# Optimization experiments

Hardware: AMD Instinct MI355X
Metric: run time of the kernel (lower is better)

Reference implementation:

```python
import jax, jax.numpy as jnp
import numpy as np

B, K, H, W, N = 256, 16, 64, 64, 1024   # batch, channels (n_ch), grid H/W, sampled sites
F_IN = 9 * K - 1                         # 3x3 neighborhood * K channels, minus center channel


def setup_inputs() -> dict:
    key = jax.random.key(0)
    ks = jax.random.split(key, 8)
    z_int = jax.random.randint(ks[0], (B, K, H, W), 0, 16, dtype=jnp.int32)
    bs = jax.random.randint(ks[1], (N,), 0, K, dtype=jnp.int32)
    ii = jax.random.randint(ks[2], (N,), 0, H, dtype=jnp.int32)
    jj = jax.random.randint(ks[3], (N,), 0, W, dtype=jnp.int32)
    W1 = jax.random.normal(ks[4], (F_IN, 128), dtype=jnp.float32) * 0.05
    b1 = jnp.zeros((128,), dtype=jnp.float32)
    W2 = jax.random.normal(ks[5], (128, 16), dtype=jnp.float32) * 0.05
    b2 = jnp.zeros((16,), dtype=jnp.float32)
    return {"z_int": z_int, "bs": bs, "ii": ii, "jj": jj,
            "W1": W1, "b1": b1, "W2": W2, "b2": b2}


def _gather_ctx(z_f, bs, ii, jj):
    # Faithful to get_context ordering: loops di, dj (each in [-1,0,1]) then b,
    # skipping (di==0, dj==0, b==bi). Flattened skip position = 4*K + bi.
    off = jnp.array([-1, 0, 1], dtype=jnp.int32)
    di = jnp.repeat(off, 3)          # [9]
    dj = jnp.tile(off, 3)            # [9]
    ni = (ii[:, None] + di[None, :]) % H   # [N, 9] toroidal wrap
    nj = (jj[:, None] + dj[None, :]) % W   # [N, 9]
    ctx = z_f[:, :, ni, nj]                # [B, K, N, 9]
    ctx = jnp.transpose(ctx, (2, 0, 3, 1)).reshape(N, B, 9 * K)  # [N, B, 9K], (di,dj) major then b
    drop = 4 * K + bs                      # [N] center-channel flat index
    idx = jnp.arange(F_IN, dtype=jnp.int32)
    keep = idx[None, :] + (idx[None, :] >= drop[:, None]).astype(jnp.int32)  # [N, F_IN]
    return jax.vmap(lambda c, k: c[:, k])(ctx, keep)  # [N, B, F_IN]


def reference(z_int, bs, ii, jj, W1, b1, W2, b2):
    z_f = z_int.astype(jnp.float32) / 15.0
    ctx = _gather_ctx(z_f, bs, ii, jj)                 # [N, B, 9K-1]
    h = jax.nn.relu(jnp.einsum('nbf,fh->nbh', ctx, W1) + b1)
    logits = jnp.einsum('nbh,hc->nbc', h, W2) + b2     # [N, B, 16]
    pred = jnp.argmax(logits, axis=-1)                 # [N, B]
    tgt = z_int[:, bs, ii, jj].T                       # [N, B]
    rate = jnp.mean((pred != tgt).astype(jnp.float32)) # np.mean of per-site mean == global mean
    return rate
```

## Files before the change

kernel.cpp:

```cpp
#include <hip/hip_runtime.h>
#include <stdint.h>

#define NB 1024
#define BB 256
#define KK 16
#define HH 64
#define WW 64
#define F_FULL 144
#define HDIM 128
#define CDIM 16
#define KPAD 160
#define APITCH 168
#define HPITCH 136
#define ABYTES (64 * APITCH * 2)

typedef __bf16 bf16x8 __attribute__((ext_vector_type(8)));
typedef float f32x4 __attribute__((ext_vector_type(4)));

#define W1T_OFF 256
#define W1T_BYTES (16 * HDIM * KPAD * 2)
#define W2B_OFF (W1T_OFF + W1T_BYTES)
#define W2B_BYTES (CDIM * HDIM * 2)
#define ZT_OFF (W2B_OFF + W2B_BYTES)

__device__ __forceinline__ unsigned short bf16_bits(float v) {
    __bf16 b = (__bf16)v;
    return __builtin_bit_cast(unsigned short, b);
}

#define TP 144
__global__ __launch_bounds__(256) void prep_kernel(
    const int* __restrict__ z, const float* __restrict__ W1,
    const float* __restrict__ W2, uint8_t* __restrict__ zt,
    unsigned short* __restrict__ W1t, unsigned short* __restrict__ W2b,
    int* __restrict__ counters) {
    int bid = blockIdx.x;
    int t = threadIdx.x;
    if (bid < 4096) {
        __shared__ uint8_t tile[32 * TP];
        int bx = bid & 127;
        int by = bid >> 7;
        int c0 = bx * 32, r0 = by * 128;
#pragma unroll
        for (int i = 0; i < 4; ++i) {
            int lin = i * 256 + t;
            int c = lin & 31;
            int rq = lin >> 5;
            uchar4 v;
            v.x = (uint8_t)z[(size_t)(r0 + rq * 4 + 0) * 4096 + c0 + c];
            v.y = (uint8_t)z[(size_t)(r0 + rq * 4 + 1) * 4096 + c0 + c];
            v.z = (uint8_t)z[(size_t)(r0 + rq * 4 + 2) * 4096 + c0 + c];
            v.w = (uint8_t)z[(size_t)(r0 + rq * 4 + 3) * 4096 + c0 + c];
            *(uchar4*)(tile + c * TP + rq * 4) = v;
        }
        __syncthreads();
        int cy = t >> 3, rx = t & 7;
        uint4 v = *(const uint4*)(tile + cy * TP + rx * 16);
        *(uint4*)(zt + (size_t)(c0 + cy) * 4096 + r0 + rx * 16) = v;
    } else if (bid < 5376) {
        int idx = (bid - 4096) * 256 + t;
        int k = idx % KPAD;
        int h = (idx / KPAD) % HDIM;
        int s = idx / (KPAD * HDIM);
        int drop = 4 * KK + s;
        float val = 0.0f;
        if (k < F_FULL && k != drop) {
            int src = k - (k > drop ? 1 : 0);
            val = W1[src * HDIM + h];
        }
        W1t[idx] = bf16_bits(val);
    } else {
        int idx = (bid - 5376) * 256 + t;
        if (idx < CDIM * HDIM) {
            int k = idx % HDIM;
            int c = idx / HDIM;
            W2b[idx] = bf16_bits(W2[k * CDIM + c]);
        }
        if (bid == 5376 && t == 0) counters[0] = 0;
    }
}

__global__ __launch_bounds__(256, 3) void main_kernel(
    const uint8_t* __restrict__ zt, const unsigned short* __restrict__ W1t,
    const float* __restrict__ b1, const unsigned short* __restrict__ W2b,
    const float* __restrict__ b2, const int* __restrict__ bs,
    const int* __restrict__ ii, const int* __restrict__ jj,
    int* __restrict__ counters) {
    __shared__ __align__(16) unsigned char smem[2 * ABYTES + 64 * 17 * 4];
    unsigned short* sA0 = (unsigned short*)smem;
    unsigned short* sA1 = (unsigned short*)(smem + ABYTES);
    float* slg = (float*)(smem + 2 * ABYTES);

    int t = threadIdx.x;
    int n = blockIdx.x;
    int wave = t >> 6, lane = t & 63;
    int l15 = lane & 15, l4 = lane >> 4;

    int in_ = ii[n], jn = jj[n], sn = bs[n];

    const unsigned short* w1s = W1t + (size_t)sn * (HDIM * KPAD);
    int n0 = wave * 32;
    bf16x8 Bf[2][5];
#pragma unroll
    for (int nt = 0; nt < 2; ++nt)
#pragma unroll
        for (int ks = 0; ks < 5; ++ks)
            Bf[nt][ks] = *(const bf16x8*)(w1s + (n0 + nt * 16 + l15) * KPAD + ks * 32 + l4 * 8);
    bf16x8 Bf2[4];
#pragma unroll
    for (int ks = 0; ks < 4; ++ks)
        Bf2[ks] = *(const bf16x8*)(W2b + l15 * HDIM + ks * 32 + l4 * 8);
    float b1v0 = b1[n0 + l15], b1v1 = b1[n0 + 16 + l15];
    float b2v = b2[l15];

    if (t < 192) {
        int b = t / 3, part = t % 3;
        *(uint4*)(sA0 + b * APITCH + F_FULL + part * 8) = make_uint4(0, 0, 0, 0);
        *(uint4*)(sA1 + b * APITCH + F_FULL + part * 8) = make_uint4(0, 0, 0, 0);
    }

    uint4 g0, g1, g2;
    auto gload = [&](int tile) {
        int b = (t & 63) + tile * 64;
        int p0 = t >> 6;
        int ni0 = (in_ + p0 / 3 - 1) & (HH - 1);
        int nj0 = (jn + p0 % 3 - 1) & (WW - 1);
        g0 = *(const uint4*)(zt + (((size_t)(ni0 * WW + nj0) * BB + b) << 4));
        int p1 = p0 + 4;
        int ni1 = (in_ + p1 / 3 - 1) & (HH - 1);
        int nj1 = (jn + p1 % 3 - 1) & (WW - 1);
        g1 = *(const uint4*)(zt + (((size_t)(ni1 * WW + nj1) * BB + b) << 4));
        if (t < 64) {
            int ni2 = (in_ + 1) & (HH - 1);
            int nj2 = (jn + 1) & (WW - 1);
            g2 = *(const uint4*)(zt + (((size_t)(ni2 * WW + nj2) * BB + b) << 4));
        }
    };
    auto gwrite = [&](unsigned short* dst) {
        int b = t & 63;
        int p0 = t >> 6;
        auto conv = [&](uint4 raw, int p) {
            const uint8_t* bytes = (const uint8_t*)&raw;
            union { __bf16 h[16]; uint4 q[2]; } u;
#pragma unroll
            for (int k = 0; k < 16; ++k)
                u.h[k] = (__bf16)((float)bytes[k] * (1.0f / 15.0f));
            uint4* d = (uint4*)(dst + b * APITCH + p * 16);
            d[0] = u.q[0];
            d[1] = u.q[1];
        };
        conv(g0, p0);
        conv(g1, p0 + 4);
        if (t < 64) conv(g2, 8);
    };

    gload(0);
    gwrite(sA0);
    int local_err = 0;

    for (int tile = 0; tile < 4; ++tile) {
        unsigned short* sA = (tile & 1) ? sA1 : sA0;
        unsigned short* sH = sA;
        unsigned short* sAnext = (tile & 1) ? sA0 : sA1;

        if (tile < 3) gload(tile + 1);
        __syncthreads();

        f32x4 acc[4][2] = {};
#pragma unroll
        for (int mt = 0; mt < 4; ++mt) {
            bf16x8 Af[5];
#pragma unroll
            for (int ks = 0; ks < 5; ++ks)
                Af[ks] = *(const bf16x8*)(sA + (mt * 16 + l15) * APITCH + ks * 32 + l4 * 8);
#pragma unroll
            for (int ks = 0; ks < 5; ++ks) {
                acc[mt][0] = __builtin_amdgcn_mfma_f32_16x16x32_bf16(Af[ks], Bf[0][ks], acc[mt][0], 0, 0, 0);
                acc[mt][1] = __builtin_amdgcn_mfma_f32_16x16x32_bf16(Af[ks], Bf[1][ks], acc[mt][1], 0, 0, 0);
            }
        }
        __syncthreads();

#pragma unroll
        for (int mt = 0; mt < 4; ++mt)
#pragma unroll
            for (int nt = 0; nt < 2; ++nt) {
                float bv = nt ? b1v1 : b1v0;
                int hcol = n0 + nt * 16 + l15;
#pragma unroll
                for (int r = 0; r < 4; ++r) {
                    int b = mt * 16 + l4 * 4 + r;
                    float v = fmaxf(acc[mt][nt][r] + bv, 0.0f);
                    sH[b * HPITCH + hcol] = bf16_bits(v);
                }
            }
        __syncthreads();

        f32x4 acc2 = {};
#pragma unroll
        for (int ks = 0; ks < 4; ++ks) {
            bf16x8 Af = *(const bf16x8*)(sH + (wave * 16 + l15) * HPITCH + ks * 32 + l4 * 8);
            acc2 = __builtin_amdgcn_mfma_f32_16x16x32_bf16(Af, Bf2[ks], acc2, 0, 0, 0);
        }
#pragma unroll
        for (int r = 0; r < 4; ++r) {
            int b = wave * 16 + l4 * 4 + r;
            slg[b * 17 + l15] = acc2[r] + b2v;
        }
        __syncthreads();

        if (t < 64) {
            float best = slg[t * 17];
            int pi = 0;
#pragma unroll
            for (int c = 1; c < CDIM; ++c) {
                float v = slg[t * 17 + c];
                if (v > best) { best = v; pi = c; }
            }
            int bglob = tile * 64 + t;
            int tgt = zt[(((size_t)(in_ * WW + jn) * BB + bglob) << 4) + sn];
            unsigned long long m = __ballot(pi != tgt);
            if (t == 0) local_err += (int)__popcll(m);
        }
        if (tile < 3) gwrite(sAnext);
    }

    if (t == 0) atomicAdd(&counters[0], local_err);
}

__global__ void finalize_kernel(const int* __restrict__ counters, float* __restrict__ out) {
    out[0] = (float)(counters[0]) / (float)(NB * BB);
}

extern "C" void kernel_launch(void* const* d_in, const int* in_sizes, int n_in,
                              void* d_out, int out_size, void* d_ws, size_t ws_size,
                              hipStream_t stream) {
    const int* z = (const int*)d_in[0];
    const int* bs = (const int*)d_in[1];
    const int* ii = (const int*)d_in[2];
    const int* jj = (const int*)d_in[3];
    const float* W1 = (const float*)d_in[4];
    const float* b1 = (const float*)d_in[5];
    const float* W2 = (const float*)d_in[6];
    const float* b2 = (const float*)d_in[7];
    float* out = (float*)d_out;

    uint8_t* ws = (uint8_t*)d_ws;
    int* counters = (int*)ws;
    unsigned short* W1t = (unsigned short*)(ws + W1T_OFF);
    unsigned short* W2b = (unsigned short*)(ws + W2B_OFF);
    uint8_t* zt = ws + ZT_OFF;

    prep_kernel<<<5384, 256, 0, stream>>>(z, W1, W2, zt, W1t, W2b, counters);
    main_kernel<<<NB, 256, 0, stream>>>(zt, W1t, b1, W2b, b2, bs, ii, jj, counters);
    finalize_kernel<<<1, 1, 0, stream>>>(counters, out);
}
```

Measured before the change: 132.7 us.

## Fuse finalize into main kernel, shuffle-based argmax, separate hidden buffer

Drops the separate finalize launch: the last block to finish, found through an atomic ticket counter, writes the output. The argmax over the 16 logits becomes a wave-level shuffle reduction, removing the logits shared-memory round trip and two block barriers per tile. A dedicated shared hidden-activation buffer removes one more barrier. Weight loads are moved after the first gather is issued so their latency overlaps, and the A pitch shrinks to 160, which may add LDS bank conflicts.

```diff
diff --git a/kernel.cpp b/kernel.cpp
--- a/kernel.cpp
+++ b/kernel.cpp
@@ -10,7 +10,7 @@
 #define HDIM 128
 #define CDIM 16
 #define KPAD 160
-#define APITCH 168
+#define APITCH 160
 #define HPITCH 136
 #define ABYTES (64 * APITCH * 2)
 
@@ -76,7 +76,7 @@
             int c = idx / HDIM;
             W2b[idx] = bf16_bits(W2[k * CDIM + c]);
         }
-        if (bid == 5376 && t == 0) counters[0] = 0;
+        if (bid == 5376 && t == 0) { counters[0] = 0; counters[1] = 0; }
     }
 }
 
@@ -85,11 +85,11 @@
     const float* __restrict__ b1, const unsigned short* __restrict__ W2b,
     const float* __restrict__ b2, const int* __restrict__ bs,
     const int* __restrict__ ii, const int* __restrict__ jj,
-    int* __restrict__ counters) {
-    __shared__ __align__(16) unsigned char smem[2 * ABYTES + 64 * 17 * 4];
+    int* __restrict__ counters, float* __restrict__ out) {
+    __shared__ __align__(16) unsigned char smem[2 * ABYTES + 64 * HPITCH * 2];
     unsigned short* sA0 = (unsigned short*)smem;
     unsigned short* sA1 = (unsigned short*)(smem + ABYTES);
-    float* slg = (float*)(smem + 2 * ABYTES);
+    unsigned short* sH = (unsigned short*)(smem + 2 * ABYTES);
 
     int t = threadIdx.x;
     int n = blockIdx.x;
@@ -97,27 +97,6 @@
     int l15 = lane & 15, l4 = lane >> 4;
 
     int in_ = ii[n], jn = jj[n], sn = bs[n];
-
-    const unsigned short* w1s = W1t + (size_t)sn * (HDIM * KPAD);
-    int n0 = wave * 32;
-    bf16x8 Bf[2][5];
-#pragma unroll
-    for (int nt = 0; nt < 2; ++nt)
-#pragma unroll
-        for (int ks = 0; ks < 5; ++ks)
-            Bf[nt][ks] = *(const bf16x8*)(w1s + (n0 + nt * 16 + l15) * KPAD + ks * 32 + l4 * 8);
-    bf16x8 Bf2[4];
-#pragma unroll
-    for (int ks = 0; ks < 4; ++ks)
-        Bf2[ks] = *(const bf16x8*)(W2b + l15 * HDIM + ks * 32 + l4 * 8);
-    float b1v0 = b1[n0 + l15], b1v1 = b1[n0 + 16 + l15];
-    float b2v = b2[l15];
-
-    if (t < 192) {
-        int b = t / 3, part = t % 3;
-        *(uint4*)(sA0 + b * APITCH + F_FULL + part * 8) = make_uint4(0, 0, 0, 0);
-        *(uint4*)(sA1 + b * APITCH + F_FULL + part * 8) = make_uint4(0, 0, 0, 0);
-    }
 
     uint4 g0, g1, g2;
     auto gload = [&](int tile) {
@@ -155,12 +134,32 @@
     };
 
     gload(0);
+
+    const unsigned short* w1s = W1t + (size_t)sn * (HDIM * KPAD);
+    int n0 = wave * 32;
+    bf16x8 Bf[2][5];
+#pragma unroll
+    for (int nt = 0; nt < 2; ++nt)
+#pragma unroll
+        for (int ks = 0; ks < 5; ++ks)
+            Bf[nt][ks] = *(const bf16x8*)(w1s + (n0 + nt * 16 + l15) * KPAD + ks * 32 + l4 * 8);
+    bf16x8 Bf2[4];
+#pragma unroll
+    for (int ks = 0; ks < 4; ++ks)
+        Bf2[ks] = *(const bf16x8*)(W2b + l15 * HDIM + ks * 32 + l4 * 8);
+    float b1v0 = b1[n0 + l15], b1v1 = b1[n0 + 16 + l15];
+    float b2v = b2[l15];
+
+    if (t < 128) {
+        unsigned short* buf = (t & 64) ? sA1 : sA0;
+        *(uint4*)(buf + (t & 63) * APITCH + F_FULL) = make_uint4(0, 0, 0, 0);
+    }
+
     gwrite(sA0);
-    int local_err = 0;
+    int werr = 0;
 
     for (int tile = 0; tile < 4; ++tile) {
         unsigned short* sA = (tile & 1) ? sA1 : sA0;
-        unsigned short* sH = sA;
         unsigned short* sAnext = (tile & 1) ? sA0 : sA1;
 
         if (tile < 3) gload(tile + 1);
@@ -179,7 +178,6 @@
                 acc[mt][1] = __builtin_amdgcn_mfma_f32_16x16x32_bf16(Af[ks], Bf[1][ks], acc[mt][1], 0, 0, 0);
             }
         }
-        __syncthreads();
 
 #pragma unroll
         for (int mt = 0; mt < 4; ++mt)
@@ -202,34 +200,40 @@
             bf16x8 Af = *(const bf16x8*)(sH + (wave * 16 + l15) * HPITCH + ks * 32 + l4 * 8);
             acc2 = __builtin_amdgcn_mfma_f32_16x16x32_bf16(Af, Bf2[ks], acc2, 0, 0, 0);
         }
+
 #pragma unroll
         for (int r = 0; r < 4; ++r) {
-            int b = wave * 16 + l4 * 4 + r;
-            slg[b * 17 + l15] = acc2[r] + b2v;
-        }
-        __syncthreads();
-
-        if (t < 64) {
-            float best = slg[t * 17];
-            int pi = 0;
-#pragma unroll
-            for (int c = 1; c < CDIM; ++c) {
-                float v = slg[t * 17 + c];
-                if (v > best) { best = v; pi = c; }
-            }
-            int bglob = tile * 64 + t;
-            int tgt = zt[(((size_t)(in_ * WW + jn) * BB + bglob) << 4) + sn];
-            unsigned long long m = __ballot(pi != tgt);
-            if (t == 0) local_err += (int)__popcll(m);
-        }
+            float v = acc2[r] + b2v;
+            int idx = l15;
+#pragma unroll
+            for (int off = 1; off < 16; off <<= 1) {
+                float ov = __shfl_xor(v, off);
+                int oi = __shfl_xor(idx, off);
+                if (ov > v || (ov == v && oi < idx)) { v = ov; idx = oi; }
+            }
+            if (l15 == 0) {
+                int bglob = tile * 64 + wave * 16 + l4 * 4 + r;
+                int tgt = zt[(((size_t)(in_ * WW + jn) * BB + bglob) << 4) + sn];
+                werr += (idx != tgt) ? 1 : 0;
+            }
+        }
+
         if (tile < 3) gwrite(sAnext);
     }
 
-    if (t == 0) atomicAdd(&counters[0], local_err);
-}
-
-__global__ void finalize_kernel(const int* __restrict__ counters, float* __restrict__ out) {
-    out[0] = (float)(counters[0]) / (float)(NB * BB);
+#pragma unroll
+    for (int off = 32; off > 0; off >>= 1) werr += __shfl_xor(werr, off);
+    if (lane == 0) atomicAdd(&counters[0], werr);
+
+    __syncthreads();
+    if (t == 0) {
+        __threadfence();
+        int old = atomicAdd(&counters[1], 1);
+        if (old == NB - 1) {
+            int total = atomicAdd(&counters[0], 0);
+            out[0] = (float)total / (float)(NB * BB);
+        }
+    }
 }
 
 extern "C" void kernel_launch(void* const* d_in, const int* in_sizes, int n_in,
@@ -252,6 +256,5 @@
     uint8_t* zt = ws + ZT_OFF;
 
     prep_kernel<<<5384, 256, 0, stream>>>(z, W1, W2, zt, W1t, W2b, counters);
-    main_kernel<<<NB, 256, 0, stream>>>(zt, W1t, b1, W2b, b2, bs, ii, jj, counters);
-    finalize_kernel<<<1, 1, 0, stream>>>(counters, out);
-}
+    main_kernel<<<NB, 256, 0, stream>>>(zt, W1t, b1, W2b, b2, bs, ii, jj, counters, out);
+}
```

Result: slower. 190.2 us (+43.3%).

## Split main kernel across eight waves with one hidden-column tile each

Applied to the files above, without the earlier changes.

Doubles the block to 512 threads so each of the eight waves computes 16 hidden columns of the first GEMM instead of 32. The 3x3 neighborhood gather is spread so each thread loads a single position, and the launch bound moves to (512, 6) to cut per-thread register pressure and raise the number of resident waves. In exchange, the second GEMM runs on only half the waves, and W2 fragments are now reloaded from global memory every tile instead of being held in registers.

```diff
diff --git a/kernel.cpp b/kernel.cpp
--- a/kernel.cpp
+++ b/kernel.cpp
@@ -80,7 +80,7 @@
     }
 }
 
-__global__ __launch_bounds__(256, 3) void main_kernel(
+__global__ __launch_bounds__(512, 6) void main_kernel(
     const uint8_t* __restrict__ zt, const unsigned short* __restrict__ W1t,
     const float* __restrict__ b1, const unsigned short* __restrict__ W2b,
     const float* __restrict__ b2, const int* __restrict__ bs,
@@ -98,38 +98,13 @@
 
     int in_ = ii[n], jn = jj[n], sn = bs[n];
 
-    const unsigned short* w1s = W1t + (size_t)sn * (HDIM * KPAD);
-    int n0 = wave * 32;
-    bf16x8 Bf[2][5];
-#pragma unroll
-    for (int nt = 0; nt < 2; ++nt)
-#pragma unroll
-        for (int ks = 0; ks < 5; ++ks)
-            Bf[nt][ks] = *(const bf16x8*)(w1s + (n0 + nt * 16 + l15) * KPAD + ks * 32 + l4 * 8);
-    bf16x8 Bf2[4];
-#pragma unroll
-    for (int ks = 0; ks < 4; ++ks)
-        Bf2[ks] = *(const bf16x8*)(W2b + l15 * HDIM + ks * 32 + l4 * 8);
-    float b1v0 = b1[n0 + l15], b1v1 = b1[n0 + 16 + l15];
-    float b2v = b2[l15];
-
-    if (t < 192) {
-        int b = t / 3, part = t % 3;
-        *(uint4*)(sA0 + b * APITCH + F_FULL + part * 8) = make_uint4(0, 0, 0, 0);
-        *(uint4*)(sA1 + b * APITCH + F_FULL + part * 8) = make_uint4(0, 0, 0, 0);
-    }
-
-    uint4 g0, g1, g2;
+    uint4 g0, g2;
     auto gload = [&](int tile) {
         int b = (t & 63) + tile * 64;
         int p0 = t >> 6;
         int ni0 = (in_ + p0 / 3 - 1) & (HH - 1);
         int nj0 = (jn + p0 % 3 - 1) & (WW - 1);
         g0 = *(const uint4*)(zt + (((size_t)(ni0 * WW + nj0) * BB + b) << 4));
-        int p1 = p0 + 4;
-        int ni1 = (in_ + p1 / 3 - 1) & (HH - 1);
-        int nj1 = (jn + p1 % 3 - 1) & (WW - 1);
-        g1 = *(const uint4*)(zt + (((size_t)(ni1 * WW + nj1) * BB + b) << 4));
         if (t < 64) {
             int ni2 = (in_ + 1) & (HH - 1);
             int nj2 = (jn + 1) & (WW - 1);
@@ -150,11 +125,26 @@
             d[1] = u.q[1];
         };
         conv(g0, p0);
-        conv(g1, p0 + 4);
         if (t < 64) conv(g2, 8);
     };
 
     gload(0);
+
+    const unsigned short* w1s = W1t + (size_t)sn * (HDIM * KPAD);
+    int n0 = wave * 16;
+    bf16x8 Bf[5];
+#pragma unroll
+    for (int ks = 0; ks < 5; ++ks)
+        Bf[ks] = *(const bf16x8*)(w1s + (n0 + l15) * KPAD + ks * 32 + l4 * 8);
+    float b1v = b1[n0 + l15];
+    float b2v = b2[l15];
+
+    if (t < 192) {
+        int b = t / 3, part = t % 3;
+        *(uint4*)(sA0 + b * APITCH + F_FULL + part * 8) = make_uint4(0, 0, 0, 0);
+        *(uint4*)(sA1 + b * APITCH + F_FULL + part * 8) = make_uint4(0, 0, 0, 0);
+    }
+
     gwrite(sA0);
     int local_err = 0;
 
@@ -166,7 +156,7 @@
         if (tile < 3) gload(tile + 1);
         __syncthreads();
 
-        f32x4 acc[4][2] = {};
+        f32x4 acc[4] = {};
 #pragma unroll
         for (int mt = 0; mt < 4; ++mt) {
             bf16x8 Af[5];
@@ -174,38 +164,33 @@
             for (int ks = 0; ks < 5; ++ks)
                 Af[ks] = *(const bf16x8*)(sA + (mt * 16 + l15) * APITCH + ks * 32 + l4 * 8);
 #pragma unroll
-            for (int ks = 0; ks < 5; ++ks) {
-                acc[mt][0] = __builtin_amdgcn_mfma_f32_16x16x32_bf16(Af[ks], Bf[0][ks], acc[mt][0], 0, 0, 0);
-                acc[mt][1] = __builtin_amdgcn_mfma_f32_16x16x32_bf16(Af[ks], Bf[1][ks], acc[mt][1], 0, 0, 0);
-            }
+            for (int ks = 0; ks < 5; ++ks)
+                acc[mt] = __builtin_amdgcn_mfma_f32_16x16x32_bf16(Af[ks], Bf[ks], acc[mt], 0, 0, 0);
         }
         __syncthreads();
 
 #pragma unroll
         for (int mt = 0; mt < 4; ++mt)
 #pragma unroll
-            for (int nt = 0; nt < 2; ++nt) {
-                float bv = nt ? b1v1 : b1v0;
-                int hcol = n0 + nt * 16 + l15;
-#pragma unroll
-                for (int r = 0; r < 4; ++r) {
-                    int b = mt * 16 + l4 * 4 + r;
-                    float v = fmaxf(acc[mt][nt][r] + bv, 0.0f);
-                    sH[b * HPITCH + hcol] = bf16_bits(v);
-                }
-            }
-        __syncthreads();
-
-        f32x4 acc2 = {};
-#pragma unroll
-        for (int ks = 0; ks < 4; ++ks) {
-            bf16x8 Af = *(const bf16x8*)(sH + (wave * 16 + l15) * HPITCH + ks * 32 + l4 * 8);
-            acc2 = __builtin_amdgcn_mfma_f32_16x16x32_bf16(Af, Bf2[ks], acc2, 0, 0, 0);
-        }
-#pragma unroll
-        for (int r = 0; r < 4; ++r) {
-            int b = wave * 16 + l4 * 4 + r;
-            slg[b * 17 + l15] = acc2[r] + b2v;
+            for (int r = 0; r < 4; ++r) {
+                int b = mt * 16 + l4 * 4 + r;
+                sH[b * HPITCH + n0 + l15] = bf16_bits(fmaxf(acc[mt][r] + b1v, 0.0f));
+            }
+        __syncthreads();
+
+        if (wave < 4) {
+            f32x4 acc2 = {};
+#pragma unroll
+            for (int ks = 0; ks < 4; ++ks) {
+                bf16x8 B2k = *(const bf16x8*)(W2b + l15 * HDIM + ks * 32 + l4 * 8);
+                bf16x8 Af = *(const bf16x8*)(sH + (wave * 16 + l15) * HPITCH + ks * 32 + l4 * 8);
+                acc2 = __builtin_amdgcn_mfma_f32_16x16x32_bf16(Af, B2k, acc2, 0, 0, 0);
+            }
+#pragma unroll
+            for (int r = 0; r < 4; ++r) {
+                int b = wave * 16 + l4 * 4 + r;
+                slg[b * 17 + l15] = acc2[r] + b2v;
+            }
         }
         __syncthreads();
 
@@ -222,6 +207,7 @@
             unsigned long long m = __ballot(pi != tgt);
             if (t == 0) local_err += (int)__popcll(m);
         }
+
         if (tile < 3) gwrite(sAnext);
     }
 
@@ -252,6 +238,6 @@
     uint8_t* zt = ws + ZT_OFF;
 
     prep_kernel<<<5384, 256, 0, stream>>>(z, W1, W2, zt, W1t, W2b, counters);
-    main_kernel<<<NB, 256, 0, stream>>>(zt, W1t, b1, W2b, b2, bs, ii, jj, counters);
+    main_kernel<<<NB, 512, 0, stream>>>(zt, W1t, b1, W2b, b2, bs, ii, jj, counters);
     finalize_kernel<<<1, 1, 0, stream>>>(counters, out);
 }
```

Measured after the change: 138.2 us. 1.04x slower.
